# Kernel optimization log

Measured on AMD Instinct MI355X. Metric: run time of the kernel, lower is better.

The kernel has to match this reference:

```python
import jax, jax.numpy as jnp
import numpy as np


def _to_box_list(x):
    # (batch, ch, nw, nh) -> (nw*nh, batch, ch)  [convert_to_box_list]
    b, c, nw, nh = x.shape
    return jnp.transpose(x, (2, 3, 0, 1)).reshape(nw * nh, b, c)


def _bilinear_sample(img, px, py):
    # img: (ch, X, Y); px: (Sx,), py: (Sy,) pixel coords; zero padding outside.
    ch, X, Y = img.shape
    x0 = jnp.floor(px); y0 = jnp.floor(py)
    wx = px - x0; wy = py - y0
    x0i = x0.astype(jnp.int32); y0i = y0.astype(jnp.int32)
    def g(xi, yi):
        xc = jnp.clip(xi, 0, X - 1); yc = jnp.clip(yi, 0, Y - 1)
        v = img[:, xc[:, None], yc[None, :]]
        m = (((xi >= 0) & (xi < X))[:, None] & ((yi >= 0) & (yi < Y))[None, :]).astype(img.dtype)
        return v * m
    return ((1 - wx)[:, None] * ((1 - wy)[None, :] * g(x0i, y0i) + wy[None, :] * g(x0i, y0i + 1))
            + wx[:, None] * ((1 - wy)[None, :] * g(x0i + 1, y0i) + wy[None, :] * g(x0i + 1, y0i + 1)))


def setup_inputs():
    key = jax.random.key(0)
    ks = jax.random.split(key, 12)
    B, CH_IN, W, H = 8, 1, 256, 256
    NW = NH = 32
    DZW, DZI, FCH, S = 4, 16, 32, 28
    feat_flat = FCH * S * S   # 25088
    out_flat = (CH_IN + 1) * S * S  # 1568
    return {
        "imgs_in": jax.random.uniform(ks[0], (B, CH_IN, W, H), jnp.float32),
        "features": jax.random.normal(ks[1], (B, FCH, W, H), jnp.float32),
        "zwhere_mu": jax.random.normal(ks[2], (B, DZW, NW, NH), jnp.float32),
        "zwhere_std": jax.random.uniform(ks[3], (B, DZW, NW, NH), jnp.float32) * 0.9 + 0.1,
        "logit_mu": jax.random.normal(ks[4], (B, 1, NW, NH), jnp.float32),
        "w_zwhere": jax.random.normal(ks[5], (4, DZW), jnp.float32) * 0.5,
        "b_zwhere": jnp.zeros((4,), jnp.float32),
        "w_enc_mu": jax.random.normal(ks[6], (DZI, feat_flat), jnp.float32) * 0.01,
        "b_enc_mu": jnp.zeros((DZI,), jnp.float32),
        "w_enc_std": jax.random.normal(ks[7], (DZI, feat_flat), jnp.float32) * 0.01,
        "b_enc_std": jnp.zeros((DZI,), jnp.float32),
        "w_dec": jax.random.normal(ks[8], (out_flat, DZI), jnp.float32) * 0.1,
        "b_dec": jnp.zeros((out_flat,), jnp.float32),
        "n_objects_max": 25,
        "cropped_size": 28,
        "size_min": 24,
        "size_max": 96,
    }


def reference(imgs_in, features, zwhere_mu, zwhere_std, logit_mu,
              w_zwhere, b_zwhere, w_enc_mu, b_enc_mu, w_enc_std, b_enc_std,
              w_dec, b_dec, n_objects_max, cropped_size, size_min, size_max):
    B, CH_IN, W, H = imgs_in.shape
    S = cropped_size
    eps = 1e-8

    # ---- box decode: Decoder1by1Linear (1x1 conv) + sigmoid + tmaps_to_bb ----
    tmaps = jax.nn.sigmoid(jnp.einsum('bcwh,oc->bowh', zwhere_mu, w_zwhere)
                           + b_zwhere[None, :, None, None])
    tx, ty, tw, th = tmaps[:, 0], tmaps[:, 1], tmaps[:, 2], tmaps[:, 3]  # (B, nw, nh)
    nw, nh = tx.shape[-2], tx.shape[-1]
    ix = jnp.arange(nw, dtype=tx.dtype)[:, None]
    iy = jnp.arange(nh, dtype=tx.dtype)[None, :]
    def tolist2(m):  # (B, nw, nh) -> (nw*nh, B)
        return jnp.transpose(m, (1, 2, 0)).reshape(nw * nh, B)
    bx_all = tolist2(W * (ix + tx) / nw)
    by_all = tolist2(H * (iy + ty) / nh)
    bw_all = tolist2(size_min + (size_max - size_min) * tw)
    bh_all = tolist2(size_min + (size_max - size_min) * th)

    # ---- prob map, Bernoulli KL vs prior 0.5, deterministic top-k (topk_only NMS) ----
    p_map = jax.nn.sigmoid(logit_mu)                                     # c_map.sample
    kl_logit = (jnp.log(2.0) + p_map * jnp.log(p_map + eps)
                + (1 - p_map) * jnp.log(1 - p_map + eps))               # c_map.kl
    p_list = _to_box_list(p_map)[..., 0]        # (n_all, B)
    logit_list = _to_box_list(logit_mu)[..., 0]
    _, idx_bk = jax.lax.top_k(p_list.T, n_objects_max)  # (B, k)
    index_top_k = idx_bk.T                              # (k, B)

    c_few = jnp.take_along_axis(p_list, index_top_k, axis=0)
    logit_few = jnp.take_along_axis(logit_list, index_top_k, axis=0)
    bx = jnp.take_along_axis(bx_all, index_top_k, axis=0)
    by = jnp.take_along_axis(by_all, index_top_k, axis=0)
    bw = jnp.take_along_axis(bw_all, index_top_k, axis=0)
    bh = jnp.take_along_axis(bh_all, index_top_k, axis=0)

    # ---- zwhere KL (diag normal vs N(0,1)), gathered at top-k boxes ----
    kl_zwhere_map = 0.5 * (zwhere_std ** 2 + zwhere_mu ** 2 - 1.0) - jnp.log(zwhere_std)
    kl_zwhere_all = _to_box_list(kl_zwhere_map)          # (n_all, B, dz)
    idx3 = jnp.broadcast_to(index_top_k[:, :, None],
                            (n_objects_max, B, kl_zwhere_all.shape[-1]))
    kl_zwhere_few = jnp.take_along_axis(kl_zwhere_all, idx3, axis=0)

    # ---- Cropper.crop: bilinear crop of UNet features at selected boxes ----
    def crop_one(img, cx, cy, cw, chh):
        t = jnp.arange(S, dtype=img.dtype) / (S - 1)
        return _bilinear_sample(img, cx - 0.5 * cw + t * cw, cy - 0.5 * chh + t * chh)
    crop_boxes = jax.vmap(crop_one, in_axes=(None, 0, 0, 0, 0))
    crop_all = jax.vmap(crop_boxes, in_axes=(0, 1, 1, 1, 1), out_axes=1)
    cropped = crop_all(features, bx, by, bw, bh)  # (k, B, FCH, S, S)

    # ---- encoder_zinstance -> z sample (= mu, noisy_sampling=False) + KL ----
    xf = cropped.reshape(n_objects_max, B, -1)
    z_mu = xf @ w_enc_mu.T + b_enc_mu
    z_std = jax.nn.softplus(xf @ w_enc_std.T + b_enc_std)
    z_sample = z_mu
    kl_zinstance = 0.5 * (z_std ** 2 + z_mu ** 2 - 1.0) - jnp.log(z_std + eps)

    # ---- decoder_zinstance -> small stuff: softplus weight ch, sigmoid img ch ----
    small_raw = (z_sample @ w_dec.T + b_dec).reshape(n_objects_max, B, CH_IN + 1, S, S)
    small = jnp.concatenate([jax.nn.softplus(small_raw[..., :1, :, :]),
                             jax.nn.sigmoid(small_raw[..., 1:, :, :])], axis=-3)

    # ---- Uncropper.uncrop: paste each small patch back at its box location ----
    def uncrop_one(sm, cx, cy, cw, chh):
        u = jnp.arange(W, dtype=sm.dtype)
        v = jnp.arange(H, dtype=sm.dtype)
        sx = (u - (cx - 0.5 * cw)) / cw * (S - 1)
        sy = (v - (cy - 0.5 * chh)) / chh * (S - 1)
        return _bilinear_sample(sm, sx, sy)
    big_stuff = jax.vmap(jax.vmap(uncrop_one))(small, bx, by, bw, bh)  # (k,B,2,W,H)

    big_weight = big_stuff[..., :1, :, :]
    big_img = big_stuff[..., 1:, :, :]
    sum_w = jnp.sum(big_weight, axis=0, keepdims=True)  # dim=-5 is box dim
    big_mask = jnp.tanh(sum_w) * (big_weight / jnp.clip(sum_w, 1e-6))
    big_mask_non = jnp.tanh(big_weight)

    return (logit_mu, logit_few, big_mask, big_mask_non, big_img,
            p_map, c_few, bx, by, bw, bh, z_sample,
            kl_logit, kl_zwhere_few, kl_zinstance)
```

## Files before the change

kernel.cpp:

```cpp
#include <hip/hip_runtime.h>
#include <math.h>

#define B 8
#define FCH 32
#define WI 256
#define HI 256
#define NW 32
#define NH 32
#define NBOX 1024
#define K 25
#define S 28
#define DZI 16
#define FEAT_FLAT (FCH*S*S)
#define FEAT4 (FEAT_FLAT/4)
#define OUT_FLAT (2*S*S)
#define SMIN 24.0f
#define SMAX 96.0f
#define BIG_SZ (K*B*WI*HI)

#define NCHUNK 49
#define CH4 128

#define O_LOGIT_MU    0
#define O_LOGIT_FEW   8192
#define O_BIG_MASK    8392
#define O_BIG_MASK_NON (O_BIG_MASK + BIG_SZ)
#define O_BIG_IMG     (O_BIG_MASK_NON + BIG_SZ)
#define O_P_MAP       (O_BIG_IMG + BIG_SZ)
#define O_C_FEW       (O_P_MAP + 8192)
#define O_BX          (O_C_FEW + 200)
#define O_BY          (O_BX + 200)
#define O_BW          (O_BY + 200)
#define O_BH          (O_BW + 200)
#define O_Z_SAMPLE    (O_BH + 200)
#define O_KL_LOGIT    (O_Z_SAMPLE + 3200)
#define O_KL_ZWHERE   (O_KL_LOGIT + 8192)
#define O_KL_ZINST    (O_KL_ZWHERE + 800)

__device__ __forceinline__ float sigmoidf_(float x) { return 1.0f / (1.0f + expf(-x)); }
__device__ __forceinline__ float softplusf_(float x) { return fmaxf(x, 0.0f) + log1pf(expf(-fabsf(x))); }
__device__ __forceinline__ float sig_fast(float x) { return 1.0f / (1.0f + __expf(-x)); }
__device__ __forceinline__ float sp_fast(float x)  { return fmaxf(x, 0.0f) + __logf(1.0f + __expf(-fabsf(x))); }
__device__ __forceinline__ float tanh_fast(float x) {
    float e = __expf(-2.0f * x);
    return (1.0f - e) / (1.0f + e);
}

__device__ __forceinline__ float tap256(const float* img, int x, int y) {
    bool in = ((unsigned)x < 256u) && ((unsigned)y < 256u);
    int xc = min(max(x, 0), 255), yc = min(max(y, 0), 255);
    float v = img[xc * 256 + yc];
    return in ? v : 0.0f;
}

__device__ __forceinline__ float tap28(const float* img, int x, int y) {
    bool in = ((unsigned)x < 28u) && ((unsigned)y < 28u);
    int xc = min(max(x, 0), 27), yc = min(max(y, 0), 27);
    float v = img[xc * 28 + yc];
    return in ? v : 0.0f;
}

__global__ void topk_kernel(const float* __restrict__ logit_mu,
                            const float* __restrict__ zmu, const float* __restrict__ zstd,
                            const float* __restrict__ w_zw, const float* __restrict__ b_zw,
                            float* __restrict__ out, float* __restrict__ ws_boxes) {
    int b = blockIdx.x;
    int lane = threadIdx.x;
    const float* lg = logit_mu + b * NBOX;
    float vals[16];
    #pragma unroll
    for (int m = 0; m < 16; ++m) vals[m] = lg[m * 64 + lane];

    unsigned taken = 0;
    int sel_idx = 0;
    for (int ks = 0; ks < K; ++ks) {
        float bv = -INFINITY; int bi = 0x7fffffff;
        #pragma unroll
        for (int m = 0; m < 16; ++m) {
            if (!(taken & (1u << m))) {
                float v = vals[m]; int idx = m * 64 + lane;
                if (v > bv || (v == bv && idx < bi)) { bv = v; bi = idx; }
            }
        }
        #pragma unroll
        for (int sh = 32; sh >= 1; sh >>= 1) {
            float ov = __shfl_xor(bv, sh);
            int   oi = __shfl_xor(bi, sh);
            if (ov > bv || (ov == bv && oi < bi)) { bv = ov; bi = oi; }
        }
        if ((bi & 63) == lane) taken |= (1u << (bi >> 6));
        if (lane == ks) sel_idx = bi;
        if (lane == 0) {
            out[O_LOGIT_FEW + ks * B + b] = bv;
            out[O_C_FEW + ks * B + b] = sigmoidf_(bv);
        }
    }

    if (lane < K) {
        int idx = sel_idx;
        int w = idx >> 5, h = idx & 31;
        float mu_c[4];
        #pragma unroll
        for (int c = 0; c < 4; ++c) mu_c[c] = zmu[((b * 4 + c) * NW + w) * NH + h];
        float t[4];
        #pragma unroll
        for (int o = 0; o < 4; ++o) {
            float a = b_zw[o];
            #pragma unroll
            for (int c = 0; c < 4; ++c) a = fmaf(mu_c[c], w_zw[o * 4 + c], a);
            t[o] = sigmoidf_(a);
        }
        float bx = (float)WI * ((float)w + t[0]) / (float)NW;
        float by = (float)HI * ((float)h + t[1]) / (float)NH;
        float bw = SMIN + (SMAX - SMIN) * t[2];
        float bh = SMIN + (SMAX - SMIN) * t[3];
        int kb = lane * B + b;
        out[O_BX + kb] = bx;
        out[O_BY + kb] = by;
        out[O_BW + kb] = bw;
        out[O_BH + kb] = bh;
        ((float4*)ws_boxes)[kb] = make_float4(bx, by, bw, bh);
        #pragma unroll
        for (int c = 0; c < 4; ++c) {
            float m = mu_c[c];
            float sd = zstd[((b * 4 + c) * NW + w) * NH + h];
            out[O_KL_ZWHERE + kb * 4 + c] = 0.5f * (sd * sd + m * m - 1.0f) - logf(sd);
        }
    }
}

__global__ __launch_bounds__(256) void crop_writer_kernel(
        const float* __restrict__ features, const float* __restrict__ ws_boxes,
        float* __restrict__ crop) {
    int c  = blockIdx.x;
    int kb = blockIdx.y;
    int b  = kb & 7;
    float4 box = ((const float4*)ws_boxes)[kb];
    float x_lo = box.x - 0.5f * box.z, y_lo = box.y - 0.5f * box.w;
    float swx = box.z * (1.0f / 27.0f), swy = box.w * (1.0f / 27.0f);
    const float* img = features + ((size_t)b * FCH + c) * (WI * HI);
    float* dst = crop + (size_t)kb * FEAT_FLAT + c * 784;

    int wave = threadIdx.x >> 6, lane = threadIdx.x & 63;
    int h  = lane >> 5;
    int iy = lane & 31;
    if (iy >= 28) return;

    float py = fmaf((float)iy, swy, y_lo);
    float y0f = floorf(py);
    float fy = py - y0f;
    int y0 = (int)y0f;
    int nits = (wave < 2) ? 4 : 3;

    float A00[4], A01[4], A10[4], A11[4], FX[4];
    int IX[4];
    #pragma unroll
    for (int it = 0; it < 4; ++it) {
        int p = wave + it * 4;
        int ix = (it < nits) ? (2 * p + h) : h;
        IX[it] = ix;
        float px = fmaf((float)ix, swx, x_lo);
        float x0f = floorf(px);
        FX[it] = px - x0f;
        int x0 = (int)x0f;
        A00[it] = tap256(img, x0, y0);
        A01[it] = tap256(img, x0, y0 + 1);
        A10[it] = tap256(img, x0 + 1, y0);
        A11[it] = tap256(img, x0 + 1, y0 + 1);
    }
    #pragma unroll
    for (int it = 0; it < 4; ++it) {
        if (it < nits) {
            float fx = FX[it];
            float v = (1.0f - fx) * ((1.0f - fy) * A00[it] + fy * A01[it])
                    +         fx  * ((1.0f - fy) * A10[it] + fy * A11[it]);
            dst[IX[it] * 28 + iy] = v;
        }
    }
}

__device__ __forceinline__ float dot4f(float4 v, float4 w, float a) {
    return fmaf(v.x, w.x, fmaf(v.y, w.y, fmaf(v.z, w.z, fmaf(v.w, w.w, a))));
}

__global__ __launch_bounds__(512) void enc_gemm_kernel(
        const float* __restrict__ crop,
        const float* __restrict__ w_mu, const float* __restrict__ w_std,
        float* __restrict__ ws_part) {
    int blk = blockIdx.x;
    int g = blk / NCHUNK, chunk = blk - g * NCHUNK;
    int wave = threadIdx.x >> 6, lane = threadIdx.x & 63;
    int base4 = chunk * CH4;
    const float4* cp4 = (const float4*)crop;

    __shared__ float4 crop_lds[8][CH4];
    {
        int t1 = threadIdx.x, t2 = threadIdx.x + 512;
        crop_lds[t1 >> 7][t1 & 127] = cp4[(size_t)(g * 8 + (t1 >> 7)) * FEAT4 + base4 + (t1 & 127)];
        crop_lds[t2 >> 7][t2 & 127] = cp4[(size_t)(g * 8 + (t2 >> 7)) * FEAT4 + base4 + (t2 & 127)];
    }

    int row = wave * 4;
    const float4* wsrc = (row < 16) ? ((const float4*)w_mu + (size_t)row * FEAT4)
                                    : ((const float4*)w_std + (size_t)(row - 16) * FEAT4);
    int i4a = base4 + lane, i4b = i4a + 64;
    float4 wa[4], wb[4];
    #pragma unroll
    for (int r = 0; r < 4; ++r) {
        wa[r] = wsrc[(size_t)r * FEAT4 + i4a];
        wb[r] = wsrc[(size_t)r * FEAT4 + i4b];
    }

    float cur[32];
    #pragma unroll
    for (int j = 0; j < 32; ++j) cur[j] = 0.0f;

    __syncthreads();

    #pragma unroll
    for (int bb = 0; bb < 8; ++bb) {
        float4 ca = crop_lds[bb][lane];
        float4 cb = crop_lds[bb][lane + 64];
        #pragma unroll
        for (int r = 0; r < 4; ++r)
            cur[r * 8 + bb] = dot4f(cb, wb[r], dot4f(ca, wa[r], cur[r * 8 + bb]));
    }

    {   bool bit = (lane & 1) != 0; float nx[16];
        #pragma unroll
        for (int j = 0; j < 16; ++j) {
            float keep = bit ? cur[2*j+1] : cur[2*j];
            float send = bit ? cur[2*j]   : cur[2*j+1];
            nx[j] = keep + __shfl_xor(send, 1);
        }
        #pragma unroll
        for (int j = 0; j < 16; ++j) cur[j] = nx[j];
    }
    {   bool bit = (lane & 2) != 0; float nx[8];
        #pragma unroll
        for (int j = 0; j < 8; ++j) {
            float keep = bit ? cur[2*j+1] : cur[2*j];
            float send = bit ? cur[2*j]   : cur[2*j+1];
            nx[j] = keep + __shfl_xor(send, 2);
        }
        #pragma unroll
        for (int j = 0; j < 8; ++j) cur[j] = nx[j];
    }
    {   bool bit = (lane & 4) != 0; float nx[4];
        #pragma unroll
        for (int j = 0; j < 4; ++j) {
            float keep = bit ? cur[2*j+1] : cur[2*j];
            float send = bit ? cur[2*j]   : cur[2*j+1];
            nx[j] = keep + __shfl_xor(send, 4);
        }
        #pragma unroll
        for (int j = 0; j < 4; ++j) cur[j] = nx[j];
    }
    {   bool bit = (lane & 8) != 0; float nx[2];
        #pragma unroll
        for (int j = 0; j < 2; ++j) {
            float keep = bit ? cur[2*j+1] : cur[2*j];
            float send = bit ? cur[2*j]   : cur[2*j+1];
            nx[j] = keep + __shfl_xor(send, 8);
        }
        cur[0] = nx[0]; cur[1] = nx[1];
    }
    {   bool bit = (lane & 16) != 0;
        float keep = bit ? cur[1] : cur[0];
        float send = bit ? cur[0] : cur[1];
        cur[0] = keep + __shfl_xor(send, 16);
    }
    float tot = cur[0] + __shfl_xor(cur[0], 32);
    if (lane < 32) {
        int kbx = g * 8 + (lane & 7);
        ws_part[((size_t)kbx * NCHUNK + chunk) * 32 + row + (lane >> 3)] = tot;
    }
}

__global__ __launch_bounds__(256) void dec_enc_kernel(
        const float* __restrict__ ws_part,
        const float* __restrict__ b_mu, const float* __restrict__ b_std,
        const float* __restrict__ w_dec, const float* __restrict__ b_dec,
        const float* __restrict__ logit_mu,
        float* __restrict__ ws_small, float* __restrict__ out) {
    int kb = blockIdx.x;
    int t = threadIdx.x;
    if (kb >= K * B) {
        int i = (kb - K * B) * 256 + t;
        float x = logit_mu[i];
        out[O_LOGIT_MU + i] = x;
        float p = sigmoidf_(x);
        out[O_P_MAP + i] = p;
        out[O_KL_LOGIT + i] = 0.69314718055994531f + p * logf(p + 1e-8f) + (1.0f - p) * logf(1.0f - p + 1e-8f);
        return;
    }
    __shared__ float zsh[DZI], spsh[DZI];
    if (t < 32) {
        float s = 0.0f;
        for (int c = 0; c < NCHUNK; ++c) s += ws_part[((size_t)kb * NCHUNK + c) * 32 + t];
        if (t < DZI) zsh[t] = s + b_mu[t];
        else         spsh[t - DZI] = s + b_std[t - DZI];
    }
    __syncthreads();
    if (t < DZI) {
        float m = zsh[t];
        float sd = softplusf_(spsh[t]);
        out[O_Z_SAMPLE + kb * DZI + t] = m;
        out[O_KL_ZINST + kb * DZI + t] = 0.5f * (sd * sd + m * m - 1.0f) - logf(sd + 1e-8f);
    }
    float z[DZI];
    #pragma unroll
    for (int j = 0; j < DZI; ++j) z[j] = zsh[j];
    for (int o = t; o < OUT_FLAT; o += 256) {
        const float4* wd = (const float4*)(w_dec + o * DZI);
        float4 w0 = wd[0], w1 = wd[1], w2 = wd[2], w3 = wd[3];
        float a = b_dec[o];
        a = fmaf(z[0], w0.x, fmaf(z[1], w0.y, fmaf(z[2], w0.z, fmaf(z[3], w0.w, a))));
        a = fmaf(z[4], w1.x, fmaf(z[5], w1.y, fmaf(z[6], w1.z, fmaf(z[7], w1.w, a))));
        a = fmaf(z[8], w2.x, fmaf(z[9], w2.y, fmaf(z[10], w2.z, fmaf(z[11], w2.w, a))));
        a = fmaf(z[12], w3.x, fmaf(z[13], w3.y, fmaf(z[14], w3.z, fmaf(z[15], w3.w, a))));
        float r = (o < 784) ? sp_fast(a) : sig_fast(a);
        ws_small[(size_t)kb * OUT_FLAT + o] = r;
    }
}

__device__ __forceinline__ void sample2_wi(const float* __restrict__ p0, float sx,
                                           float y_lo, float ih, int v0,
                                           float* __restrict__ w, float* __restrict__ im) {
    const float* p1 = p0 + 784;
    float x0f = floorf(sx); float fx = sx - x0f; int x0 = (int)x0f;
    #pragma unroll
    for (int q = 0; q < 2; ++q) {
        float sy = ((float)(v0 + q) - y_lo) * ih;
        float wv = 0.0f, iv = 0.0f;
        if (sy > -1.0f && sy < 28.0f) {
            float y0f = floorf(sy); float fy = sy - y0f; int y0 = (int)y0f;
            float a00 = tap28(p0, x0, y0),     a01 = tap28(p0, x0, y0 + 1);
            float a10 = tap28(p0, x0 + 1, y0), a11 = tap28(p0, x0 + 1, y0 + 1);
            wv = (1.0f - fx) * ((1.0f - fy) * a00 + fy * a01)
               +         fx  * ((1.0f - fy) * a10 + fy * a11);
            float c00 = tap28(p1, x0, y0),     c01 = tap28(p1, x0, y0 + 1);
            float c10 = tap28(p1, x0 + 1, y0), c11 = tap28(p1, x0 + 1, y0 + 1);
            iv = (1.0f - fx) * ((1.0f - fy) * c00 + fy * c01)
               +         fx  * ((1.0f - fy) * c10 + fy * c11);
        }
        w[q] = wv; im[q] = iv;
    }
}

__device__ __forceinline__ void sample2_w(const float* __restrict__ p0, float sx,
                                          float y_lo, float ih, int v0,
                                          float* __restrict__ w) {
    float x0f = floorf(sx); float fx = sx - x0f; int x0 = (int)x0f;
    #pragma unroll
    for (int q = 0; q < 2; ++q) {
        float sy = ((float)(v0 + q) - y_lo) * ih;
        float wv = 0.0f;
        if (sy > -1.0f && sy < 28.0f) {
            float y0f = floorf(sy); float fy = sy - y0f; int y0 = (int)y0f;
            float a00 = tap28(p0, x0, y0),     a01 = tap28(p0, x0, y0 + 1);
            float a10 = tap28(p0, x0 + 1, y0), a11 = tap28(p0, x0 + 1, y0 + 1);
            wv = (1.0f - fx) * ((1.0f - fy) * a00 + fy * a01)
               +         fx  * ((1.0f - fy) * a10 + fy * a11);
        }
        w[q] = wv;
    }
}

__global__ __launch_bounds__(256) void uncrop_kernel(const float* __restrict__ ws_small,
                                                     const float* __restrict__ ws_boxes,
                                                     float* __restrict__ out) {
    int blk = blockIdx.x;
    int b = blk >> 7;
    int ug = blk & 127;
    int t = threadIdx.x;
    int u = ug * 2 + (t >> 7);
    int v0 = (t & 127) << 1;

    __shared__ float4 bt[K];
    if (t < K) {
        float4 bx = ((const float4*)ws_boxes)[t * B + b];
        bt[t] = make_float4(bx.x - 0.5f * bx.z, bx.y - 0.5f * bx.w, 27.0f / bx.z, 27.0f / bx.w);
    }
    __syncthreads();

    float fu = (float)u;
    float sum[2] = {0.0f, 0.0f};
    #pragma unroll 2
    for (int k = 0; k < K; ++k) {
        float4 bb = bt[k];
        float sx = (fu - bb.x) * bb.z;
        float w[2] = {0, 0}, im[2] = {0, 0};
        if (sx > -1.0f && sx < 28.0f) {
            const float* p0 = ws_small + (size_t)(k * B + b) * OUT_FLAT;
            sample2_wi(p0, sx, bb.y, bb.w, v0, w, im);
        }
        sum[0] += w[0]; sum[1] += w[1];
        size_t base = (((size_t)(k * B + b) * 256 + u) * 256 + v0);
        *(float2*)(out + O_BIG_IMG + base) = make_float2(im[0], im[1]);
        *(float2*)(out + O_BIG_MASK_NON + base) = make_float2(tanh_fast(w[0]), tanh_fast(w[1]));
    }
    float sc[2];
    sc[0] = tanh_fast(sum[0]) / fmaxf(sum[0], 1e-6f);
    sc[1] = tanh_fast(sum[1]) / fmaxf(sum[1], 1e-6f);
    #pragma unroll 2
    for (int k = 0; k < K; ++k) {
        float4 bb = bt[k];
        float sx = (fu - bb.x) * bb.z;
        float w[2] = {0, 0};
        if (sx > -1.0f && sx < 28.0f) {
            const float* p0 = ws_small + (size_t)(k * B + b) * OUT_FLAT;
            sample2_w(p0, sx, bb.y, bb.w, v0, w);
        }
        size_t base = (((size_t)(k * B + b) * 256 + u) * 256 + v0);
        *(float2*)(out + O_BIG_MASK + base) = make_float2(w[0] * sc[0], w[1] * sc[1]);
    }
}

extern "C" void kernel_launch(void* const* d_in, const int* in_sizes, int n_in,
                              void* d_out, int out_size, void* d_ws, size_t ws_size,
                              hipStream_t stream) {
    const float* features = (const float*)d_in[1];
    const float* zwhere_mu = (const float*)d_in[2];
    const float* zwhere_std = (const float*)d_in[3];
    const float* logit_mu = (const float*)d_in[4];
    const float* w_zwhere = (const float*)d_in[5];
    const float* b_zwhere = (const float*)d_in[6];
    const float* w_enc_mu = (const float*)d_in[7];
    const float* b_enc_mu = (const float*)d_in[8];
    const float* w_enc_std = (const float*)d_in[9];
    const float* b_enc_std = (const float*)d_in[10];
    const float* w_dec = (const float*)d_in[11];
    const float* b_dec = (const float*)d_in[12];
    float* out = (float*)d_out;

    float* ws_boxes = (float*)d_ws;
    float* ws_part  = ws_boxes + 200 * 4;
    float* ws_small = ws_part + 200 * NCHUNK * 32;
    float* ws_crop  = out + O_BIG_IMG;

    hipLaunchKernelGGL(topk_kernel, dim3(B), dim3(64), 0, stream,
                       logit_mu, zwhere_mu, zwhere_std, w_zwhere, b_zwhere, out, ws_boxes);
    hipLaunchKernelGGL(crop_writer_kernel, dim3(FCH, 200), dim3(256), 0, stream,
                       features, ws_boxes, ws_crop);
    hipLaunchKernelGGL(enc_gemm_kernel, dim3(25 * NCHUNK), dim3(512), 0, stream,
                       ws_crop, w_enc_mu, w_enc_std, ws_part);
    hipLaunchKernelGGL(dec_enc_kernel, dim3(K * B + 32), dim3(256), 0, stream,
                       ws_part, b_enc_mu, b_enc_std, w_dec, b_dec, logit_mu, ws_small, out);
    hipLaunchKernelGGL(uncrop_kernel, dim3(B * 128), dim3(256), 0, stream,
                       ws_small, ws_boxes, out);
}
```

Measured before the change: 109.7 us.

## Stage crop source footprint in LDS with float4 loads before bilinear sampling

The crop kernel now splits each channel crop into 7 strips of 4 output rows. Each 128-thread block first loads the covering source region (up to 13 rows by 112 columns) from global memory into shared memory with aligned float4 loads, then does the bilinear taps from LDS. This replaces four scattered global gathers per output pixel with coalesced, reused loads. The cost is a block barrier, a launch grid seven times larger, and fixed LDS bounds that assume the box size stays within 96 pixels.

```diff
diff --git a/kernel.cpp b/kernel.cpp
--- a/kernel.cpp
+++ b/kernel.cpp
@@ -21,6 +21,10 @@
 #define NCHUNK 49
 #define CH4 128
 
+#define STRIPS 7
+#define SROWS 13
+#define SCOLS 112
+
 #define O_LOGIT_MU    0
 #define O_LOGIT_FEW   8192
 #define O_BIG_MASK    8392
@@ -46,13 +50,6 @@
     return (1.0f - e) / (1.0f + e);
 }
 
-__device__ __forceinline__ float tap256(const float* img, int x, int y) {
-    bool in = ((unsigned)x < 256u) && ((unsigned)y < 256u);
-    int xc = min(max(x, 0), 255), yc = min(max(y, 0), 255);
-    float v = img[xc * 256 + yc];
-    return in ? v : 0.0f;
-}
-
 __device__ __forceinline__ float tap28(const float* img, int x, int y) {
     bool in = ((unsigned)x < 28u) && ((unsigned)y < 28u);
     int xc = min(max(x, 0), 27), yc = min(max(y, 0), 27);
@@ -129,53 +126,70 @@
     }
 }
 
-__global__ __launch_bounds__(256) void crop_writer_kernel(
+__global__ __launch_bounds__(128) void crop_writer_kernel(
         const float* __restrict__ features, const float* __restrict__ ws_boxes,
         float* __restrict__ crop) {
-    int c  = blockIdx.x;
+    int blk = blockIdx.x;
+    int s = blk % STRIPS;
+    int c = blk / STRIPS;
     int kb = blockIdx.y;
     int b  = kb & 7;
     float4 box = ((const float4*)ws_boxes)[kb];
     float x_lo = box.x - 0.5f * box.z, y_lo = box.y - 0.5f * box.w;
     float swx = box.z * (1.0f / 27.0f), swy = box.w * (1.0f / 27.0f);
     const float* img = features + ((size_t)b * FCH + c) * (WI * HI);
-    float* dst = crop + (size_t)kb * FEAT_FLAT + c * 784;
-
-    int wave = threadIdx.x >> 6, lane = threadIdx.x & 63;
-    int h  = lane >> 5;
-    int iy = lane & 31;
-    if (iy >= 28) return;
-
-    float py = fmaf((float)iy, swy, y_lo);
-    float y0f = floorf(py);
-    float fy = py - y0f;
-    int y0 = (int)y0f;
-    int nits = (wave < 2) ? 4 : 3;
-
-    float A00[4], A01[4], A10[4], A11[4], FX[4];
-    int IX[4];
-    #pragma unroll
-    for (int it = 0; it < 4; ++it) {
-        int p = wave + it * 4;
-        int ix = (it < nits) ? (2 * p + h) : h;
-        IX[it] = ix;
+
+    int y0min = (int)floorf(y_lo);
+    int y1 = (int)floorf(fmaf(27.0f, swy, y_lo)) + 1;
+    int ya = y0min & ~3;
+    int ncol4 = ((y1 - ya) >> 2) + 1;
+
+    int x0min = (int)floorf(fmaf((float)(4 * s), swx, x_lo));
+    int x1 = (int)floorf(fmaf((float)(4 * s + 3), swx, x_lo)) + 1;
+    int nrows = x1 - x0min + 1;
+
+    __shared__ float lds[SROWS][SCOLS];
+
+    int t = threadIdx.x;
+    int lane = t & 63;
+    int half = t >> 6;
+    for (int r = half; r < nrows; r += 2) {
+        int gx = x0min + r;
+        bool xin = (unsigned)gx < 256u;
+        if (lane < ncol4) {
+            int yb = ya + (lane << 2);
+            float4 v = make_float4(0.0f, 0.0f, 0.0f, 0.0f);
+            if (xin) {
+                const float* row = img + gx * 256;
+                if (yb >= 0 && yb + 3 < 256) {
+                    v = *(const float4*)(row + yb);
+                } else {
+                    v.x = ((unsigned)(yb + 0) < 256u) ? row[yb + 0] : 0.0f;
+                    v.y = ((unsigned)(yb + 1) < 256u) ? row[yb + 1] : 0.0f;
+                    v.z = ((unsigned)(yb + 2) < 256u) ? row[yb + 2] : 0.0f;
+                    v.w = ((unsigned)(yb + 3) < 256u) ? row[yb + 3] : 0.0f;
+                }
+            }
+            *(float4*)&lds[r][lane << 2] = v;
+        }
+    }
+    __syncthreads();
+
+    int iy = t & 31;
+    int ixl = t >> 5;
+    if (iy < 28) {
+        int ix = s * 4 + ixl;
         float px = fmaf((float)ix, swx, x_lo);
-        float x0f = floorf(px);
-        FX[it] = px - x0f;
-        int x0 = (int)x0f;
-        A00[it] = tap256(img, x0, y0);
-        A01[it] = tap256(img, x0, y0 + 1);
-        A10[it] = tap256(img, x0 + 1, y0);
-        A11[it] = tap256(img, x0 + 1, y0 + 1);
-    }
-    #pragma unroll
-    for (int it = 0; it < 4; ++it) {
-        if (it < nits) {
-            float fx = FX[it];
-            float v = (1.0f - fx) * ((1.0f - fy) * A00[it] + fy * A01[it])
-                    +         fx  * ((1.0f - fy) * A10[it] + fy * A11[it]);
-            dst[IX[it] * 28 + iy] = v;
-        }
+        float x0f = floorf(px); float fx = px - x0f;
+        int r = (int)x0f - x0min;
+        float py = fmaf((float)iy, swy, y_lo);
+        float y0f = floorf(py); float fy = py - y0f;
+        int j = (int)y0f - ya;
+        float a00 = lds[r][j],     a01 = lds[r][j + 1];
+        float a10 = lds[r + 1][j], a11 = lds[r + 1][j + 1];
+        float v = (1.0f - fx) * ((1.0f - fy) * a00 + fy * a01)
+                +         fx  * ((1.0f - fy) * a10 + fy * a11);
+        crop[(size_t)kb * FEAT_FLAT + c * 784 + ix * 28 + iy] = v;
     }
 }
 
@@ -441,7 +455,7 @@
 
     hipLaunchKernelGGL(topk_kernel, dim3(B), dim3(64), 0, stream,
                        logit_mu, zwhere_mu, zwhere_std, w_zwhere, b_zwhere, out, ws_boxes);
-    hipLaunchKernelGGL(crop_writer_kernel, dim3(FCH, 200), dim3(256), 0, stream,
+    hipLaunchKernelGGL(crop_writer_kernel, dim3(STRIPS * FCH, 200), dim3(128), 0, stream,
                        features, ws_boxes, ws_crop);
     hipLaunchKernelGGL(enc_gemm_kernel, dim3(25 * NCHUNK), dim3(512), 0, stream,
                        ws_crop, w_enc_mu, w_enc_std, ws_part);
```

New measurement: 127.3 us. 1.16x slower.

## Separate crop bilinear into row interpolation in shared memory then column taps

Applied to the files above, without the earlier changes.

The crop kernel now loads two full 256-wide source rows per output row with coalesced float4 reads, interpolates along x into a shared 28x256 buffer, then does the y interpolation from shared memory. This replaces four scattered gathers per output pixel. It reads whole rows (1 KB each) even though only a narrow window is needed, so global traffic can rise for small boxes, and it adds 28 KB of shared memory per block, which may limit occupancy.

```diff
diff --git a/kernel.cpp b/kernel.cpp
--- a/kernel.cpp
+++ b/kernel.cpp
@@ -46,13 +46,6 @@
     return (1.0f - e) / (1.0f + e);
 }
 
-__device__ __forceinline__ float tap256(const float* img, int x, int y) {
-    bool in = ((unsigned)x < 256u) && ((unsigned)y < 256u);
-    int xc = min(max(x, 0), 255), yc = min(max(y, 0), 255);
-    float v = img[xc * 256 + yc];
-    return in ? v : 0.0f;
-}
-
 __device__ __forceinline__ float tap28(const float* img, int x, int y) {
     bool in = ((unsigned)x < 28u) && ((unsigned)y < 28u);
     int xc = min(max(x, 0), 27), yc = min(max(y, 0), 27);
@@ -141,40 +134,46 @@
     const float* img = features + ((size_t)b * FCH + c) * (WI * HI);
     float* dst = crop + (size_t)kb * FEAT_FLAT + c * 784;
 
-    int wave = threadIdx.x >> 6, lane = threadIdx.x & 63;
-    int h  = lane >> 5;
-    int iy = lane & 31;
-    if (iy >= 28) return;
-
-    float py = fmaf((float)iy, swy, y_lo);
-    float y0f = floorf(py);
-    float fy = py - y0f;
-    int y0 = (int)y0f;
-    int nits = (wave < 2) ? 4 : 3;
-
-    float A00[4], A01[4], A10[4], A11[4], FX[4];
-    int IX[4];
-    #pragma unroll
-    for (int it = 0; it < 4; ++it) {
-        int p = wave + it * 4;
-        int ix = (it < nits) ? (2 * p + h) : h;
-        IX[it] = ix;
+    __shared__ float G[28][256];
+
+    int t = threadIdx.x;
+    int wave = t >> 6, lane = t & 63;
+
+    #pragma unroll
+    for (int p = 0; p < 7; ++p) {
+        int ix = p * 4 + wave;
         float px = fmaf((float)ix, swx, x_lo);
         float x0f = floorf(px);
-        FX[it] = px - x0f;
+        float fx = px - x0f;
         int x0 = (int)x0f;
-        A00[it] = tap256(img, x0, y0);
-        A01[it] = tap256(img, x0, y0 + 1);
-        A10[it] = tap256(img, x0 + 1, y0);
-        A11[it] = tap256(img, x0 + 1, y0 + 1);
-    }
-    #pragma unroll
-    for (int it = 0; it < 4; ++it) {
-        if (it < nits) {
-            float fx = FX[it];
-            float v = (1.0f - fx) * ((1.0f - fy) * A00[it] + fy * A01[it])
-                    +         fx  * ((1.0f - fy) * A10[it] + fy * A11[it]);
-            dst[IX[it] * 28 + iy] = v;
+        float4 a = make_float4(0.0f, 0.0f, 0.0f, 0.0f);
+        float4 bb = a;
+        const float* r0 = img + x0 * 256 + (lane << 2);
+        if ((unsigned)x0 < 256u)       a  = *(const float4*)r0;
+        if ((unsigned)(x0 + 1) < 256u) bb = *(const float4*)(r0 + 256);
+        float4 g;
+        g.x = (1.0f - fx) * a.x + fx * bb.x;
+        g.y = (1.0f - fx) * a.y + fx * bb.y;
+        g.z = (1.0f - fx) * a.z + fx * bb.z;
+        g.w = (1.0f - fx) * a.w + fx * bb.w;
+        *(float4*)&G[ix][lane << 2] = g;
+    }
+    __syncthreads();
+
+    int iy = t & 31, grp = t >> 5;
+    if (iy < 28) {
+        float py = fmaf((float)iy, swy, y_lo);
+        float y0f = floorf(py);
+        float fy = py - y0f;
+        int j = (int)y0f;
+        float m0 = ((unsigned)j < 256u) ? 1.0f : 0.0f;
+        float m1 = ((unsigned)(j + 1) < 256u) ? 1.0f : 0.0f;
+        int j0 = min(max(j, 0), 255);
+        int j1 = min(max(j + 1, 0), 255);
+        for (int ix = grp; ix < 28; ix += 8) {
+            float a = G[ix][j0] * m0;
+            float bv = G[ix][j1] * m1;
+            dst[ix * 28 + iy] = (1.0f - fy) * a + fy * bv;
         }
     }
 }
```

Result: slower. 124.8 us (+13.7%).
